# Optimization experiments

Hardware: AMD Instinct MI355X
Metric: run time of the kernel (lower is better)

## Reference

```python
import jax, jax.numpy as jnp
import numpy as np

N_TH1 = 30
LB = 1e-20
UB = 1e20
LB_EXP = -20.0
UB_EXP = 20.0


def make_directions(n_th1):
    # Reproduces the TF __init__ direction sampling on the sphere.
    n_th2 = 2 * (n_th1 - 1) + 1
    th1 = np.linspace(-np.pi / 2, np.pi / 2, n_th1)
    th2 = np.linspace(-np.pi, np.pi, n_th2)
    c1, s1 = np.cos(th1), np.sin(th1)
    c2, s2 = np.cos(th2), np.sin(th2)
    dx = np.outer(c1[1:-1], c2[:-1])          # [n_th1-2, n_th2-1]
    dy = np.outer(c1[1:-1], s2[:-1])
    dz = np.broadcast_to(s1[1:-1, None], dx.shape)
    mid = np.stack([dx, dy, dz], -1).reshape(-1, 3)
    poles = np.array([[c1[0] * c2[0], c1[0] * s2[0], s1[0]],
                      [c1[-1] * c2[0], c1[-1] * s2[0], s1[-1]]])
    return np.concatenate([mid, poles], 0).astype(np.float32)  # [D, 3]


def setup_inputs() -> dict:
    key = jax.random.key(0)
    k1, k2, k3 = jax.random.split(key, 3)
    vertices = jax.random.normal(k1, (8, 64, 32, 3), jnp.float32)
    # smoothness is a p-norm exponent; realistic range [2, 20]
    smoothness = 2.0 + 18.0 * jax.random.uniform(k2, (8, 64), jnp.float32)
    pointcloud = jax.random.normal(k3, (8, 2048, 3), jnp.float32)
    return {"vertices": vertices, "smoothness": smoothness, "pointcloud": pointcloud}


def _spt_forward(vertices, smoothness):
    dirs = jnp.asarray(make_directions(N_TH1))            # [D, 3]
    B, P = vertices.shape[0], vertices.shape[1]
    mean_v = jnp.mean(vertices, axis=2, keepdims=True)    # [B,P,1,3]
    local_v = vertices - mean_v                           # [B,P,V,3]

    # z = <v, x> for every vertex/direction pair -> [B,P,V,D]
    z = jnp.einsum('bpvc,dc->bpvd', local_v, dirs)
    zm = jnp.maximum(z, 0.0)
    p = smoothness[:, :, None, None]                      # [B,P,1,1]

    # dynamic rescaling k = 10^ceil(...) to keep zm^p in fp range
    zm_max = jnp.max(zm, axis=2, keepdims=True)           # [B,P,1,D]
    zm_log = jnp.log(zm_max) / jnp.log(10.0)              # = max over V of log10(zm)
    exponent = zm_log * p
    lk = jnp.where(exponent < LB_EXP, (-15.0 - exponent) / p, 0.0)
    k = 10.0 ** jnp.clip(jnp.ceil(lk), 0.0, UB_EXP)       # [B,P,1,D]
    k = jax.lax.stop_gradient(k)                          # ceil has zero grad anyway

    zm = zm * k
    pos = zm > 0
    # clip(zm^p, lb, ub) - (zm==0)*lb  ==  where(zm>0, clip(zm^p,lb,ub), 0)
    zm_p = jnp.where(pos, jnp.clip(jnp.where(pos, zm, 1.0) ** p, LB, UB), 0.0)
    sum_zm_p = jnp.sum(zm_p, axis=2, keepdims=True)       # [B,P,1,D]
    spos = sum_zm_p > 0
    h = jnp.where(spos, jnp.clip(jnp.where(spos, sum_zm_p, 1.0) ** (1.0 / p), LB, UB), LB)

    # dh/dz = clip((zm/h)^(p-1), lb, ub)
    ratio = zm / h                                        # [B,P,V,D]
    rpos = ratio > 0
    dhdz = jnp.where(rpos, jnp.clip(jnp.where(rpos, ratio, 1.0) ** (p - 1.0), LB, UB), LB)
    # dh/dx = dhdz^T @ vertices -> surface points
    dhdx = jnp.einsum('bpvd,bpvc->bpdc', dhdz, local_v)   # [B,P,D,3]
    surf = dhdx + mean_v                                  # broadcast [B,P,1,3]

    h_out = jnp.clip(h / k, -UB, UB)                      # [B,P,1,D]
    h_out = jnp.transpose(h_out, (0, 1, 3, 2))            # [B,P,D,1]
    local_dirs = jnp.broadcast_to(dirs[None, None], (B, P) + dirs.shape)
    direction_h = jnp.concatenate([local_dirs, h_out], axis=-1)  # [B,P,D,4]
    points = surf.reshape(B, -1, 3)                       # [B, P*D, 3]
    mean_out = mean_v.reshape(B, P, 3)
    return points, direction_h, mean_out, local_v


def reference(vertices, smoothness, pointcloud):
    points, direction_h, mean_out, local_v = _spt_forward(vertices, smoothness)
    B, P = vertices.shape[0], vertices.shape[1]
    # overlap / retraction loops are truncated in the source; placeholders
    overlap = jnp.zeros((B, P, 1), jnp.float32)
    retraction = jnp.zeros((B, P, 1), jnp.float32)
    return (points, direction_h, overlap, retraction, mean_out, local_v)
```

## Files before the change

### kernel.cpp

```cpp
#include <hip/hip_runtime.h>
#include <math.h>

#define NBP 512
#define VV 32
#define DD 1626
#define DHALF 813

#define O_POINTS 0
#define O_DIRH   2497536
#define O_OVER   5827584
#define O_RETR   5828096
#define O_MEAN   5828608
#define O_LOCAL  5830144

#define L10_2 0.3010299956639812f
#define L2_10 3.321928094887362f
#define LH_MIN -66.43856189774725f

__device__ __forceinline__ float fexp2(float x) {
  return __builtin_amdgcn_exp2f(x);
}

__device__ __forceinline__ void make_dir_fast(int d, float& x, float& y, float& z) {
  if (d < 1624) {
    const int i1 = d / 58 + 1;
    const int i2 = d - (i1 - 1) * 58;
    const float STEP = 0.10833078115826873f;
    const float th1 = -1.5707963267948966f + (float)i1 * STEP;
    const float th2 = -3.14159265358979323846f + (float)i2 * STEP;
    const float s1 = __sinf(th1);
    const float c1 = __cosf(th1);
    const float s2 = __sinf(th2);
    const float c2 = __cosf(th2);
    x = c1 * c2; y = c1 * s2; z = s1;
  } else if (d == 1624) {
    x = -6.123234e-17f; y = -7.49880e-33f; z = -1.0f;
  } else {
    x = -6.123234e-17f; y = -7.49880e-33f; z = 1.0f;
  }
}

#define RL(x, i) __uint_as_float(__builtin_amdgcn_readlane(__float_as_uint(x), (i)))

#define DECL_CHUNK(b)                                                       \
  const float cx_##b##_0 = RL(lvx, 4*b+0), cx_##b##_1 = RL(lvx, 4*b+1),     \
              cx_##b##_2 = RL(lvx, 4*b+2), cx_##b##_3 = RL(lvx, 4*b+3);     \
  const float cy_##b##_0 = RL(lvy, 4*b+0), cy_##b##_1 = RL(lvy, 4*b+1),     \
              cy_##b##_2 = RL(lvy, 4*b+2), cy_##b##_3 = RL(lvy, 4*b+3);     \
  const float cz_##b##_0 = RL(lvz, 4*b+0), cz_##b##_1 = RL(lvz, 4*b+1),     \
              cz_##b##_2 = RL(lvz, 4*b+2), cz_##b##_3 = RL(lvz, 4*b+3);

#define P1CH(b) {                                                           \
  float z0 = fmaxf(fmaf(cx_##b##_0, dx, fmaf(cy_##b##_0, dy, cz_##b##_0 * dz)), 0.f); \
  float z1 = fmaxf(fmaf(cx_##b##_1, dx, fmaf(cy_##b##_1, dy, cz_##b##_1 * dz)), 0.f); \
  float z2 = fmaxf(fmaf(cx_##b##_2, dx, fmaf(cy_##b##_2, dy, cz_##b##_2 * dz)), 0.f); \
  float z3 = fmaxf(fmaf(cx_##b##_3, dx, fmaf(cy_##b##_3, dy, cz_##b##_3 * dz)), 0.f); \
  zm0 = fmaxf(zm0, z0); zm1 = fmaxf(zm1, z1);                               \
  zm2 = fmaxf(zm2, z2); zm3 = fmaxf(zm3, z3); }

#define P2CH(b) {                                                           \
  float z0 = fmaxf(fmaf(cx_##b##_0, dx, fmaf(cy_##b##_0, dy, cz_##b##_0 * dz)), 0.f); \
  float z1 = fmaxf(fmaf(cx_##b##_1, dx, fmaf(cy_##b##_1, dy, cz_##b##_1 * dz)), 0.f); \
  float z2 = fmaxf(fmaf(cx_##b##_2, dx, fmaf(cy_##b##_2, dy, cz_##b##_2 * dz)), 0.f); \
  float z3 = fmaxf(fmaf(cx_##b##_3, dx, fmaf(cy_##b##_3, dy, cz_##b##_3 * dz)), 0.f); \
  float w0 = fexp2(fmaf(pm1, __log2f(z0), A));                              \
  float w1 = fexp2(fmaf(pm1, __log2f(z1), A));                              \
  float w2 = fexp2(fmaf(pm1, __log2f(z2), A));                              \
  float w3 = fexp2(fmaf(pm1, __log2f(z3), A));                              \
  s0 += w0 * z0;  s1 += w1 * z1;                                            \
  s2 += w2 * z2;  s3 += w3 * z3;                                            \
  ax = fmaf(w0, cx_##b##_0, fmaf(w1, cx_##b##_1, fmaf(w2, cx_##b##_2, fmaf(w3, cx_##b##_3, ax)))); \
  ay = fmaf(w0, cy_##b##_0, fmaf(w1, cy_##b##_1, fmaf(w2, cy_##b##_2, fmaf(w3, cy_##b##_3, ay)))); \
  az = fmaf(w0, cz_##b##_0, fmaf(w1, cz_##b##_1, fmaf(w2, cz_##b##_2, fmaf(w3, cz_##b##_3, az)))); }

#define PROCESS(IDX) do {                                                   \
  const int d = dbase + (IDX);                                              \
  float dx, dy, dz;                                                         \
  make_dir_fast(d, dx, dy, dz);                                             \
  float zm0 = 0.f, zm1 = 0.f, zm2 = 0.f, zm3 = 0.f;                         \
  P1CH(0) P1CH(1) P1CH(2) P1CH(3) P1CH(4) P1CH(5) P1CH(6) P1CH(7)           \
  const float zmax = fmaxf(fmaxf(zm0, zm1), fmaxf(zm2, zm3));               \
  const float expo = __log2f(zmax) * plt;                                   \
  float kc = 0.f;                                                           \
  if (expo < -20.f) kc = fminf(fmaxf(ceilf((-15.f - expo) * inv_p), 0.f), 20.f); \
  const float kcl = kc * L2_10;                                             \
  const float A   = p * kcl;                                                \
  float s0 = 0.f, s1 = 0.f, s2 = 0.f, s3 = 0.f;                             \
  float ax = 0.f, ay = 0.f, az = 0.f;                                       \
  P2CH(0) P2CH(1) P2CH(2) P2CH(3) P2CH(4) P2CH(5) P2CH(6) P2CH(7)           \
  const float ssum = (s0 + s1) + (s2 + s3);                                 \
  float lh = LH_MIN, C2 = 0.f;                                              \
  if (ssum > 0.f) {                                                         \
    lh = inv_p * __log2f(ssum);                                             \
    C2 = fexp2(-fmaf(pm1, lh, kcl));                                        \
  }                                                                         \
  const int pbase = bp * DD + d;                                            \
  out[O_POINTS + pbase * 3 + 0] = fmaf(C2, ax, mx);                         \
  out[O_POINTS + pbase * 3 + 1] = fmaf(C2, ay, my);                         \
  out[O_POINTS + pbase * 3 + 2] = fmaf(C2, az, mz);                         \
  float4 dvh = make_float4(dx, dy, dz, fexp2(lh - kcl));                    \
  ((float4*)(out + O_DIRH))[pbase] = dvh;                                   \
} while (0)

__global__ __launch_bounds__(256) void spt_kernel(
    const float* __restrict__ vertices,
    const float* __restrict__ smooth,
    float* __restrict__ out)
{
  const int bp   = blockIdx.x;
  const int half = blockIdx.y;
  const int tid  = threadIdx.x;

  const int dbase = half * DHALF;

  const int v = tid & 31;
  const float* vp = vertices + bp * (VV * 3) + v * 3;
  const float vx = vp[0], vy = vp[1], vz = vp[2];
  float sx = vx, sy = vy, sz = vz;
#pragma unroll
  for (int m = 16; m >= 1; m >>= 1) {
    sx += __shfl_xor(sx, m);
    sy += __shfl_xor(sy, m);
    sz += __shfl_xor(sz, m);
  }
  const float mx = sx * (1.0f / 32.0f);
  const float my = sy * (1.0f / 32.0f);
  const float mz = sz * (1.0f / 32.0f);

  const float lvx = vx - mx;
  const float lvy = vy - my;
  const float lvz = vz - mz;

  DECL_CHUNK(0) DECL_CHUNK(1) DECL_CHUNK(2) DECL_CHUNK(3)
  DECL_CHUNK(4) DECL_CHUNK(5) DECL_CHUNK(6) DECL_CHUNK(7)

  if (half == 1) {
    if (tid < VV) {
      out[O_LOCAL + bp * (VV * 3) + tid * 3 + 0] = lvx;
      out[O_LOCAL + bp * (VV * 3) + tid * 3 + 1] = lvy;
      out[O_LOCAL + bp * (VV * 3) + tid * 3 + 2] = lvz;
    }
    if (tid == 96) {
      out[O_MEAN + bp * 3 + 0] = mx;
      out[O_MEAN + bp * 3 + 1] = my;
      out[O_MEAN + bp * 3 + 2] = mz;
      out[O_OVER + bp] = 0.f;
      out[O_RETR + bp] = 0.f;
    }
  }

  const float p     = smooth[bp];
  const float inv_p = 1.0f / p;
  const float pm1   = p - 1.0f;
  const float plt   = p * L10_2;

  PROCESS(tid);
  PROCESS(256 + tid);
  PROCESS(512 + tid);
  if (tid < DHALF - 768) PROCESS(768 + tid);
}

extern "C" void kernel_launch(void* const* d_in, const int* in_sizes, int n_in,
                              void* d_out, int out_size, void* d_ws, size_t ws_size,
                              hipStream_t stream) {
  const float* vertices = (const float*)d_in[0];
  const float* smooth   = (const float*)d_in[1];
  float* out = (float*)d_out;

  spt_kernel<<<dim3(NBP, 2), 256, 0, stream>>>(vertices, smooth, out);
}
```

Baseline: 75.69 us.

## Fuse max and weighted-sum passes, recomputing only when rescaling is needed

```diff
diff --git a/kernel.cpp b/kernel.cpp
--- a/kernel.cpp
+++ b/kernel.cpp
@@ -50,57 +50,22 @@
   const float cz_##b##_0 = RL(lvz, 4*b+0), cz_##b##_1 = RL(lvz, 4*b+1),     \
               cz_##b##_2 = RL(lvz, 4*b+2), cz_##b##_3 = RL(lvz, 4*b+3);
 
-#define P1CH(b) {                                                           \
+#define MCH(b) {                                                            \
   float z0 = fmaxf(fmaf(cx_##b##_0, dx, fmaf(cy_##b##_0, dy, cz_##b##_0 * dz)), 0.f); \
   float z1 = fmaxf(fmaf(cx_##b##_1, dx, fmaf(cy_##b##_1, dy, cz_##b##_1 * dz)), 0.f); \
   float z2 = fmaxf(fmaf(cx_##b##_2, dx, fmaf(cy_##b##_2, dy, cz_##b##_2 * dz)), 0.f); \
   float z3 = fmaxf(fmaf(cx_##b##_3, dx, fmaf(cy_##b##_3, dy, cz_##b##_3 * dz)), 0.f); \
   zm0 = fmaxf(zm0, z0); zm1 = fmaxf(zm1, z1);                               \
-  zm2 = fmaxf(zm2, z2); zm3 = fmaxf(zm3, z3); }
-
-#define P2CH(b) {                                                           \
-  float z0 = fmaxf(fmaf(cx_##b##_0, dx, fmaf(cy_##b##_0, dy, cz_##b##_0 * dz)), 0.f); \
-  float z1 = fmaxf(fmaf(cx_##b##_1, dx, fmaf(cy_##b##_1, dy, cz_##b##_1 * dz)), 0.f); \
-  float z2 = fmaxf(fmaf(cx_##b##_2, dx, fmaf(cy_##b##_2, dy, cz_##b##_2 * dz)), 0.f); \
-  float z3 = fmaxf(fmaf(cx_##b##_3, dx, fmaf(cy_##b##_3, dy, cz_##b##_3 * dz)), 0.f); \
-  float w0 = fexp2(fmaf(pm1, __log2f(z0), A));                              \
-  float w1 = fexp2(fmaf(pm1, __log2f(z1), A));                              \
-  float w2 = fexp2(fmaf(pm1, __log2f(z2), A));                              \
-  float w3 = fexp2(fmaf(pm1, __log2f(z3), A));                              \
+  zm2 = fmaxf(zm2, z2); zm3 = fmaxf(zm3, z3);                               \
+  float w0 = fexp2(fmaf(pm1, __log2f(z0), 0.0f));                           \
+  float w1 = fexp2(fmaf(pm1, __log2f(z1), 0.0f));                           \
+  float w2 = fexp2(fmaf(pm1, __log2f(z2), 0.0f));                           \
+  float w3 = fexp2(fmaf(pm1, __log2f(z3), 0.0f));                           \
   s0 += w0 * z0;  s1 += w1 * z1;                                            \
   s2 += w2 * z2;  s3 += w3 * z3;                                            \
   ax = fmaf(w0, cx_##b##_0, fmaf(w1, cx_##b##_1, fmaf(w2, cx_##b##_2, fmaf(w3, cx_##b##_3, ax)))); \
   ay = fmaf(w0, cy_##b##_0, fmaf(w1, cy_##b##_1, fmaf(w2, cy_##b##_2, fmaf(w3, cy_##b##_3, ay)))); \
   az = fmaf(w0, cz_##b##_0, fmaf(w1, cz_##b##_1, fmaf(w2, cz_##b##_2, fmaf(w3, cz_##b##_3, az)))); }
-
-#define PROCESS(IDX) do {                                                   \
-  const int d = dbase + (IDX);                                              \
-  float dx, dy, dz;                                                         \
-  make_dir_fast(d, dx, dy, dz);                                             \
-  float zm0 = 0.f, zm1 = 0.f, zm2 = 0.f, zm3 = 0.f;                         \
-  P1CH(0) P1CH(1) P1CH(2) P1CH(3) P1CH(4) P1CH(5) P1CH(6) P1CH(7)           \
-  const float zmax = fmaxf(fmaxf(zm0, zm1), fmaxf(zm2, zm3));               \
-  const float expo = __log2f(zmax) * plt;                                   \
-  float kc = 0.f;                                                           \
-  if (expo < -20.f) kc = fminf(fmaxf(ceilf((-15.f - expo) * inv_p), 0.f), 20.f); \
-  const float kcl = kc * L2_10;                                             \
-  const float A   = p * kcl;                                                \
-  float s0 = 0.f, s1 = 0.f, s2 = 0.f, s3 = 0.f;                             \
-  float ax = 0.f, ay = 0.f, az = 0.f;                                       \
-  P2CH(0) P2CH(1) P2CH(2) P2CH(3) P2CH(4) P2CH(5) P2CH(6) P2CH(7)           \
-  const float ssum = (s0 + s1) + (s2 + s3);                                 \
-  float lh = LH_MIN, C2 = 0.f;                                              \
-  if (ssum > 0.f) {                                                         \
-    lh = inv_p * __log2f(ssum);                                             \
-    C2 = fexp2(-fmaf(pm1, lh, kcl));                                        \
-  }                                                                         \
-  const int pbase = bp * DD + d;                                            \
-  out[O_POINTS + pbase * 3 + 0] = fmaf(C2, ax, mx);                         \
-  out[O_POINTS + pbase * 3 + 1] = fmaf(C2, ay, my);                         \
-  out[O_POINTS + pbase * 3 + 2] = fmaf(C2, az, mz);                         \
-  float4 dvh = make_float4(dx, dy, dz, fexp2(lh - kcl));                    \
-  ((float4*)(out + O_DIRH))[pbase] = dvh;                                   \
-} while (0)
 
 __global__ __launch_bounds__(256) void spt_kernel(
     const float* __restrict__ vertices,
@@ -154,10 +119,67 @@
   const float pm1   = p - 1.0f;
   const float plt   = p * L10_2;
 
-  PROCESS(tid);
-  PROCESS(256 + tid);
-  PROCESS(512 + tid);
-  if (tid < DHALF - 768) PROCESS(768 + tid);
+#pragma unroll 1
+  for (int rep = 0; rep < 4; ++rep) {
+    const int idx = rep * 256 + tid;
+    if (idx >= DHALF) break;
+    const int d = dbase + idx;
+    float dx, dy, dz;
+    make_dir_fast(d, dx, dy, dz);
+
+    float zm0 = 0.f, zm1 = 0.f, zm2 = 0.f, zm3 = 0.f;
+    float s0 = 0.f, s1 = 0.f, s2 = 0.f, s3 = 0.f;
+    float ax = 0.f, ay = 0.f, az = 0.f;
+    MCH(0) MCH(1) MCH(2) MCH(3) MCH(4) MCH(5) MCH(6) MCH(7)
+    const float zmax = fmaxf(fmaxf(zm0, zm1), fmaxf(zm2, zm3));
+
+    float kcl = 0.f;
+    const float expo = __log2f(zmax) * plt;
+    if (expo < -20.f) {
+      const float kc = fminf(fmaxf(ceilf((-15.f - expo) * inv_p), 0.f), 20.f);
+      kcl = kc * L2_10;
+      const float A = p * kcl;
+      s0 = s1 = s2 = s3 = 0.f;
+      ax = ay = az = 0.f;
+#pragma unroll 1
+      for (int j = 0; j < 8; ++j) {
+        const float X0 = RL(lvx, 4*j+0), X1 = RL(lvx, 4*j+1),
+                    X2 = RL(lvx, 4*j+2), X3 = RL(lvx, 4*j+3);
+        const float Y0 = RL(lvy, 4*j+0), Y1 = RL(lvy, 4*j+1),
+                    Y2 = RL(lvy, 4*j+2), Y3 = RL(lvy, 4*j+3);
+        const float Z0 = RL(lvz, 4*j+0), Z1 = RL(lvz, 4*j+1),
+                    Z2 = RL(lvz, 4*j+2), Z3 = RL(lvz, 4*j+3);
+        float z0 = fmaxf(fmaf(X0, dx, fmaf(Y0, dy, Z0 * dz)), 0.f);
+        float z1 = fmaxf(fmaf(X1, dx, fmaf(Y1, dy, Z1 * dz)), 0.f);
+        float z2 = fmaxf(fmaf(X2, dx, fmaf(Y2, dy, Z2 * dz)), 0.f);
+        float z3 = fmaxf(fmaf(X3, dx, fmaf(Y3, dy, Z3 * dz)), 0.f);
+        float w0 = fexp2(fmaf(pm1, __log2f(z0), A));
+        float w1 = fexp2(fmaf(pm1, __log2f(z1), A));
+        float w2 = fexp2(fmaf(pm1, __log2f(z2), A));
+        float w3 = fexp2(fmaf(pm1, __log2f(z3), A));
+        s0 += w0 * z0;  s1 += w1 * z1;
+        s2 += w2 * z2;  s3 += w3 * z3;
+        ax = fmaf(w0, X0, fmaf(w1, X1, fmaf(w2, X2, fmaf(w3, X3, ax))));
+        ay = fmaf(w0, Y0, fmaf(w1, Y1, fmaf(w2, Y2, fmaf(w3, Y3, ay))));
+        az = fmaf(w0, Z0, fmaf(w1, Z1, fmaf(w2, Z2, fmaf(w3, Z3, az))));
+      }
+    }
+    const float ssum = (s0 + s1) + (s2 + s3);
+
+    float lh = LH_MIN, C2 = 0.f;
+    if (ssum > 0.f) {
+      lh = inv_p * __log2f(ssum);
+      C2 = fexp2(-fmaf(pm1, lh, kcl));
+    }
+
+    const int pbase = bp * DD + d;
+    out[O_POINTS + pbase * 3 + 0] = fmaf(C2, ax, mx);
+    out[O_POINTS + pbase * 3 + 1] = fmaf(C2, ay, my);
+    out[O_POINTS + pbase * 3 + 2] = fmaf(C2, az, mz);
+
+    float4 dvh = make_float4(dx, dy, dz, fexp2(lh - kcl));
+    ((float4*)(out + O_DIRH))[pbase] = dvh;
+  }
 }
 
 extern "C" void kernel_launch(void* const* d_in, const int* in_sizes, int n_in,
```

New measurement: 76.06 us. No clear change (+0.5%).
